# Optimization experiments

Hardware: AMD Instinct MI355X
Metric: run time of the kernel (lower is better)

The kernel has to match this reference:

```python
import jax, jax.numpy as jnp
import numpy as np

B, V, L, H, E, META = 2048, 4096, 10, 512, 256, 15
TAU = 1.2
SOS = 0
EOS = 0


def setup_inputs() -> dict:
    key = jax.random.key(0)
    ks = jax.random.split(key, 8)
    hidden_state = jax.random.normal(ks[0], (B, META), jnp.float32)
    W_in = jax.random.normal(ks[1], (META, H), jnp.float32) * 0.1
    b_in = jnp.zeros((H,), jnp.float32)
    embedding = jax.random.normal(ks[2], (V, E), jnp.float32) * 0.1
    W_ih = jax.random.normal(ks[3], (4 * H, E), jnp.float32) * (1.0 / np.sqrt(E))
    W_hh = jax.random.normal(ks[4], (4 * H, H), jnp.float32) * (1.0 / np.sqrt(H))
    b_ih = jnp.zeros((4 * H,), jnp.float32)
    # forget-gate bias initialized to 1 (reset_parameters)
    b_hh = jnp.zeros((4 * H,), jnp.float32).at[H:2 * H].set(1.0)
    W_out = jax.random.normal(ks[5], (H, V), jnp.float32) * 0.02
    b_out = jnp.zeros((V,), jnp.float32)
    u = jax.random.uniform(ks[6], (L, B, V), jnp.float32, 1e-8, 1.0 - 1e-8)
    gumbel = -jnp.log(-jnp.log(u))
    return {"hidden_state": hidden_state, "W_in": W_in, "b_in": b_in,
            "embedding": embedding, "W_ih": W_ih, "W_hh": W_hh,
            "b_ih": b_ih, "b_hh": b_hh, "W_out": W_out, "b_out": b_out,
            "gumbel": gumbel}


def reference(hidden_state, W_in, b_in, embedding, W_ih, W_hh, b_ih, b_hh,
              W_out, b_out, gumbel):
    initial_length = L + 1
    h0 = hidden_state @ W_in + b_in              # [B,H] input_module (meta)
    c0 = jnp.zeros_like(h0)
    tok0 = jnp.zeros((B, V), jnp.float32).at[:, SOS].set(1.0)  # one-hot sos
    sl0 = jnp.full((B,), initial_length, jnp.int32)

    def step(carry, xs):
        h, c, tok, sl = carry
        i, g = xs
        emb = tok @ embedding                                  # [B,E]
        gates = emb @ W_ih.T + b_ih + h @ W_hh.T + b_hh        # [B,4H]
        ig, fg, gg, og = jnp.split(gates, 4, axis=1)
        c = jax.nn.sigmoid(fg) * c + jax.nn.sigmoid(ig) * jnp.tanh(gg)
        h = jax.nn.sigmoid(og) * jnp.tanh(c)
        logits = h @ W_out + b_out                             # [B,V]
        logp = jax.nn.log_softmax(logits, axis=1)
        p = jnp.exp(logp)
        ent = -jnp.sum(p * logp, axis=1)                       # Categorical entropy
        # gumbel_softmax(p, tau, hard=True): softmax((log p + g)/tau), straight-through
        y = jax.nn.softmax((logp + g) / TAU, axis=1)
        hard = jax.nn.one_hot(jnp.argmax(y, axis=1), V, dtype=y.dtype)
        tok_new = jax.lax.stop_gradient(hard - y) + y
        mask = (hard[:, EOS] == 1.0) & (sl == initial_length)
        sl = jnp.where(mask, i + 2, sl)  # seq_pos = i+1, set to seq_pos+1
        return (h, c, tok_new, sl), (tok_new, emb, ent)

    (_, _, _, seq_lengths), (toks, embeds, ents) = jax.lax.scan(
        step, (h0, c0, tok0, sl0), (jnp.arange(L, dtype=jnp.int32), gumbel))
    output = jnp.concatenate([tok0[:, None, :], jnp.transpose(toks, (1, 0, 2))], axis=1)  # [B,L+1,V]
    embeds_out = jnp.transpose(embeds, (1, 0, 2))              # [B,L,E]
    entropy = jnp.mean(jnp.sum(ents, axis=0)) / L
    sentence_probability = jnp.zeros((B, V), jnp.float32)      # only filled in eval mode
    return output, seq_lengths, entropy, embeds_out, sentence_probability
```

## Files before the change

kernel.cpp:

```cpp
#include <hip/hip_runtime.h>
#include <hip/hip_bf16.h>
#include <math.h>

typedef unsigned short u16;
typedef __attribute__((ext_vector_type(8))) short bf16x8;
typedef __attribute__((ext_vector_type(4))) float f32x4;

#define B_    2048
#define V_    4096
#define L_    10
#define H_    512
#define E_    256
#define META_ 15
#define H4_   2048
#define EOS_  0
#define INIT_LEN_ (L_ + 1)

constexpr size_t OUT_SL  = (size_t)B_ * (L_ + 1) * V_;
constexpr size_t OUT_ENT = OUT_SL + B_;
constexpr size_t OUT_EMB = OUT_ENT + 1;
constexpr size_t OUT_SP  = OUT_EMB + (size_t)B_ * L_ * E_;

constexpr size_t WS_E2G     = 0;
constexpr size_t WS_BIG     = WS_E2G + (size_t)V_ * H4_;
constexpr size_t WS_C       = WS_BIG + (size_t)B_ * V_;
constexpr size_t WS_F32_END = WS_C + (size_t)B_ * H_;
constexpr size_t U_WOUT_HI  = 0;
constexpr size_t U_WOUT_LO  = U_WOUT_HI + (size_t)V_ * H_;
constexpr size_t U_WHH_HI   = U_WOUT_LO + (size_t)V_ * H_;
constexpr size_t U_WHH_LO   = U_WHH_HI + (size_t)H4_ * H_;
constexpr size_t U_HHI      = U_WHH_LO + (size_t)H4_ * H_;
constexpr size_t U_HLO      = U_HHI + (size_t)B_ * H_;
constexpr size_t U_END      = U_HLO + (size_t)B_ * H_;

__device__ __forceinline__ u16 f2bf(float f) {
    union { __hip_bfloat16 b; u16 u; } cv; cv.b = __float2bfloat16(f); return cv.u;
}
__device__ __forceinline__ float bf2f(u16 u) {
    union { u16 u; __hip_bfloat16 b; } cv; cv.u = u; return __bfloat162float(cv.b);
}

__device__ __forceinline__ void gld16(const u16* g, void* l) {
    __builtin_amdgcn_global_load_lds(
        (const __attribute__((address_space(1))) unsigned int*)g,
        (__attribute__((address_space(3))) unsigned int*)l, 16, 0, 0);
}

template <int EPI>
__global__ __launch_bounds__(256)
void gemm_mfma(const u16* __restrict__ Ah, const u16* __restrict__ Al,
               const u16* __restrict__ Bh, const u16* __restrict__ Bl,
               float* __restrict__ C, int N, int K,
               const float* __restrict__ bias, const int* __restrict__ tokidx,
               const float* __restrict__ e2g)
{
    __shared__ u16 As[2][128][32];
    __shared__ u16 Bs[2][128][32];
    const int tid  = threadIdx.x;
    const int lane = tid & 63;
    const int wave = tid >> 6;
    const int wm = wave >> 1, wn = wave & 1;
    const int col0 = blockIdx.x * 128;
    const int row0 = blockIdx.y * 128;

    const int srow = tid >> 2;
    const int scol = (tid & 3) * 8;
    const size_t aoff = (size_t)(row0 + srow) * K + scol;
    const size_t boff = (size_t)(col0 + srow) * K + scol;
    const size_t skip = (size_t)64 * K;

    u16* lA0 = &As[0][0][0];
    u16* lA1 = &As[1][0][0];
    u16* lB0 = &Bs[0][0][0];
    u16* lB1 = &Bs[1][0][0];
    const int d0 = tid * 8;
    const int d1 = d0 + 2048;

    f32x4 acc[4][4] = {};
    const int fr = lane & 15;
    const int kq = lane >> 4;

    for (int k0 = 0; k0 < K; k0 += 32) {
        __syncthreads();
        gld16(Ah + aoff + k0,        lA0 + d0);
        gld16(Ah + aoff + k0 + skip, lA0 + d1);
        gld16(Al + aoff + k0,        lA1 + d0);
        gld16(Al + aoff + k0 + skip, lA1 + d1);
        gld16(Bh + boff + k0,        lB0 + d0);
        gld16(Bh + boff + k0 + skip, lB0 + d1);
        gld16(Bl + boff + k0,        lB1 + d0);
        gld16(Bl + boff + k0 + skip, lB1 + d1);
        __syncthreads();

        bf16x8 ah[4], al[4], bh[4], bl[4];
#pragma unroll
        for (int i = 0; i < 4; ++i) {
            ah[i] = *(const bf16x8*)&As[0][wm * 64 + i * 16 + fr][kq * 8];
            al[i] = *(const bf16x8*)&As[1][wm * 64 + i * 16 + fr][kq * 8];
            bh[i] = *(const bf16x8*)&Bs[0][wn * 64 + i * 16 + fr][kq * 8];
            bl[i] = *(const bf16x8*)&Bs[1][wn * 64 + i * 16 + fr][kq * 8];
        }
#pragma unroll
        for (int mi = 0; mi < 4; ++mi)
#pragma unroll
            for (int ni = 0; ni < 4; ++ni) {
                acc[mi][ni] = __builtin_amdgcn_mfma_f32_16x16x32_bf16(ah[mi], bh[ni], acc[mi][ni], 0, 0, 0);
                acc[mi][ni] = __builtin_amdgcn_mfma_f32_16x16x32_bf16(ah[mi], bl[ni], acc[mi][ni], 0, 0, 0);
                acc[mi][ni] = __builtin_amdgcn_mfma_f32_16x16x32_bf16(al[mi], bh[ni], acc[mi][ni], 0, 0, 0);
            }
    }

    const int ccol = col0 + wn * 64 + fr;
#pragma unroll
    for (int mi = 0; mi < 4; ++mi) {
#pragma unroll
        for (int r = 0; r < 4; ++r) {
            const int grow = row0 + wm * 64 + mi * 16 + kq * 4 + r;
            float* cp = C + (size_t)grow * N + ccol;
            const float* ep = (EPI == 1) ? (e2g + (size_t)tokidx[grow] * H4_ + ccol)
                                         : nullptr;
#pragma unroll
            for (int ni = 0; ni < 4; ++ni) {
                float v = acc[mi][ni][r];
                if (EPI == 1) v += ep[ni * 16];
                if (EPI == 2) v += bias[ccol + ni * 16];
                cp[ni * 16] = v;
            }
        }
    }
}

template <int EPI>
__global__ __launch_bounds__(256)
void gemm_nt(const float* __restrict__ A, const float* __restrict__ Bm,
             float* __restrict__ C, int M, int N, int K,
             const float* __restrict__ bias0, const float* __restrict__ bias1)
{
    __shared__ float As[8][132];
    __shared__ float Bs[8][132];
    const int tid  = threadIdx.x;
    const int col0 = blockIdx.x * 128;
    const int row0 = blockIdx.y * 128;
    const int tx = tid & 15;
    const int ty = tid >> 4;
    const int lrow = tid >> 1;
    const int lkq  = (tid & 1) * 4;

    const float* Aptr = A + (size_t)(row0 + lrow) * K + lkq;
    const float* Bptr = Bm + (size_t)(col0 + lrow) * K + lkq;

    float acc[8][8] = {};

    for (int k0 = 0; k0 < K; k0 += 8) {
        float4 av = *(const float4*)(Aptr + k0);
        float4 bv = *(const float4*)(Bptr + k0);
        __syncthreads();
        As[lkq + 0][lrow] = av.x; As[lkq + 1][lrow] = av.y;
        As[lkq + 2][lrow] = av.z; As[lkq + 3][lrow] = av.w;
        Bs[lkq + 0][lrow] = bv.x; Bs[lkq + 1][lrow] = bv.y;
        Bs[lkq + 2][lrow] = bv.z; Bs[lkq + 3][lrow] = bv.w;
        __syncthreads();
#pragma unroll
        for (int kk = 0; kk < 8; ++kk) {
            float4 a0 = *(const float4*)&As[kk][ty * 8];
            float4 a1 = *(const float4*)&As[kk][ty * 8 + 4];
            float4 b0 = *(const float4*)&Bs[kk][tx * 8];
            float4 b1 = *(const float4*)&Bs[kk][tx * 8 + 4];
            float ar[8] = {a0.x, a0.y, a0.z, a0.w, a1.x, a1.y, a1.z, a1.w};
            float br[8] = {b0.x, b0.y, b0.z, b0.w, b1.x, b1.y, b1.z, b1.w};
#pragma unroll
            for (int r = 0; r < 8; ++r)
#pragma unroll
                for (int cc = 0; cc < 8; ++cc)
                    acc[r][cc] = fmaf(ar[r], br[cc], acc[r][cc]);
        }
    }

    const int ccol = col0 + tx * 8;
#pragma unroll
    for (int r = 0; r < 8; ++r) {
        const int grow = row0 + ty * 8 + r;
        float* cp = C + (size_t)grow * N + ccol;
#pragma unroll
        for (int cc = 0; cc < 8; ++cc) {
            float v = acc[r][cc];
            if (EPI == 0) v += bias0[ccol + cc] + bias1[ccol + cc];
            acc[r][cc] = v;
        }
        *(float4*)(cp)     = make_float4(acc[r][0], acc[r][1], acc[r][2], acc[r][3]);
        *(float4*)(cp + 4) = make_float4(acc[r][4], acc[r][5], acc[r][6], acc[r][7]);
    }
}

__global__ __launch_bounds__(256)
void split_wout(const float* __restrict__ W_out, u16* __restrict__ hiT,
                u16* __restrict__ loT)
{
    __shared__ float t[32][33];
    const int v0 = blockIdx.x * 32, k0 = blockIdx.y * 32;
    const int x = threadIdx.x & 31, y = threadIdx.x >> 5;
    for (int yy = y; yy < 32; yy += 8)
        t[yy][x] = W_out[(size_t)(k0 + yy) * V_ + v0 + x];
    __syncthreads();
    for (int yy = y; yy < 32; yy += 8) {
        const float v = t[x][yy];
        const u16 h = f2bf(v);
        hiT[(size_t)(v0 + yy) * H_ + k0 + x] = h;
        loT[(size_t)(v0 + yy) * H_ + k0 + x] = f2bf(v - bf2f(h));
    }
}

__global__ __launch_bounds__(256)
void split_mat(const float* __restrict__ X, u16* __restrict__ hi,
               u16* __restrict__ lo)
{
    const int i = blockIdx.x * 256 + threadIdx.x;
    float4 v = ((const float4*)X)[i];
    const u16 h0 = f2bf(v.x), h1 = f2bf(v.y), h2 = f2bf(v.z), h3 = f2bf(v.w);
    ((ushort4*)hi)[i] = make_ushort4(h0, h1, h2, h3);
    ((ushort4*)lo)[i] = make_ushort4(f2bf(v.x - bf2f(h0)), f2bf(v.y - bf2f(h1)),
                                     f2bf(v.z - bf2f(h2)), f2bf(v.w - bf2f(h3)));
}

__global__ __launch_bounds__(256)
void h0_kernel(const float* __restrict__ hs, const float* __restrict__ W_in,
               const float* __restrict__ b_in, u16* __restrict__ h_hi,
               u16* __restrict__ h_lo, float* __restrict__ c)
{
    const int idx = blockIdx.x * 256 + threadIdx.x;
    const int b = idx >> 9, j = idx & 511;
    float acc = b_in[j];
#pragma unroll
    for (int e = 0; e < META_; ++e)
        acc = fmaf(hs[b * META_ + e], W_in[e * H_ + j], acc);
    const u16 hh = f2bf(acc);
    h_hi[idx] = hh;
    h_lo[idx] = f2bf(acc - bf2f(hh));
    c[idx] = 0.f;
}

__global__ __launch_bounds__(256)
void init_outputs(float* __restrict__ out, int* __restrict__ tok,
                  int* __restrict__ sl, float* __restrict__ ents)
{
    const int tid = blockIdx.x * 256 + threadIdx.x;
    {
        const int b = tid >> 10;
        const int q = tid & 1023;
        float4 z = make_float4(0.f, 0.f, 0.f, 0.f);
        if (q == 0) z.x = 1.0f;
        ((float4*)out)[(size_t)b * ((L_ + 1) * V_ / 4) + q] = z;
    }
    for (size_t t = tid; t < (size_t)B_ * V_; t += (size_t)gridDim.x * 256)
        out[OUT_SP + t] = 0.f;
    if (tid < B_) { tok[tid] = 0; sl[tid] = INIT_LEN_; ents[tid] = 0.f; }
}

__global__ __launch_bounds__(256)
void lstm_cell(const float* __restrict__ gates, u16* __restrict__ h_hi,
               u16* __restrict__ h_lo, float* __restrict__ c,
               const float* __restrict__ embedding, const int* __restrict__ tok,
               float* __restrict__ out, int step)
{
    const int idx = blockIdx.x * 256 + threadIdx.x;
    const int b = idx >> 9, j = idx & 511;
    const size_t g0 = (size_t)b * H4_;
    const float ig = gates[g0 + j];
    const float fg = gates[g0 + H_ + j];
    const float gg = gates[g0 + 2 * H_ + j];
    const float og = gates[g0 + 3 * H_ + j];
    const float si = 1.f / (1.f + expf(-ig));
    const float sf = 1.f / (1.f + expf(-fg));
    const float so = 1.f / (1.f + expf(-og));
    const float cn = sf * c[idx] + si * tanhf(gg);
    c[idx] = cn;
    const float hv = so * tanhf(cn);
    const u16 hh = f2bf(hv);
    h_hi[idx] = hh;
    h_lo[idx] = f2bf(hv - bf2f(hh));
    if (j < E_)
        out[OUT_EMB + ((size_t)b * L_ + step) * E_ + j] =
            embedding[(size_t)tok[b] * E_ + j];
}

__global__ __launch_bounds__(256)
void softmax_step(const float* __restrict__ logits, const float* __restrict__ gumbel,
                  float* __restrict__ out, int* __restrict__ tok,
                  int* __restrict__ sl, float* __restrict__ ents, int step)
{
    const int b   = blockIdx.x;
    const int tid = threadIdx.x;
    const float* lrow = logits + (size_t)b * V_;
    const float* grow = gumbel + ((size_t)step * B_ + b) * V_;
    __shared__ float lsm[V_];
    __shared__ float red_m[4], red_bv[4], red_s[4], red_t[4];
    __shared__ int   red_bi[4];
    __shared__ float s_M;
    __shared__ int   s_bi;

    float m = -3.4e38f, bv = -3.4e38f;
    int bi = 0x7fffffff;
    for (int q = tid; q < V_ / 4; q += 256) {
        float4 l4 = ((const float4*)lrow)[q];
        float4 g4 = ((const float4*)grow)[q];
        ((float4*)lsm)[q] = l4;
        m = fmaxf(m, fmaxf(fmaxf(l4.x, l4.y), fmaxf(l4.z, l4.w)));
        float p; const int i4 = q * 4;
        p = l4.x + g4.x; if (p > bv) { bv = p; bi = i4; }
        p = l4.y + g4.y; if (p > bv) { bv = p; bi = i4 + 1; }
        p = l4.z + g4.z; if (p > bv) { bv = p; bi = i4 + 2; }
        p = l4.w + g4.w; if (p > bv) { bv = p; bi = i4 + 3; }
    }
#pragma unroll
    for (int off = 32; off > 0; off >>= 1) {
        m = fmaxf(m, __shfl_down(m, off));
        float obv = __shfl_down(bv, off);
        int   obi = __shfl_down(bi, off);
        if (obv > bv || (obv == bv && obi < bi)) { bv = obv; bi = obi; }
    }
    const int wave = tid >> 6, lane = tid & 63;
    if (lane == 0) { red_m[wave] = m; red_bv[wave] = bv; red_bi[wave] = bi; }
    __syncthreads();
    if (tid == 0) {
        m = red_m[0]; bv = red_bv[0]; bi = red_bi[0];
        for (int w = 1; w < 4; ++w) {
            m = fmaxf(m, red_m[w]);
            if (red_bv[w] > bv || (red_bv[w] == bv && red_bi[w] < bi)) {
                bv = red_bv[w]; bi = red_bi[w];
            }
        }
        s_M = m; s_bi = bi;
    }
    __syncthreads();
    const float M = s_M;
    const int amax = s_bi;

    float s = 0.f, t = 0.f;
    for (int q = tid; q < V_; q += 256) {
        const float l = lsm[q];
        const float e = __expf(l - M);
        s += e; t += e * l;
    }
#pragma unroll
    for (int off = 32; off > 0; off >>= 1) {
        s += __shfl_down(s, off);
        t += __shfl_down(t, off);
    }
    if (lane == 0) { red_s[wave] = s; red_t[wave] = t; }

    float* orow = out + ((size_t)b * (L_ + 1) + step + 1) * V_;
    const float4 z4 = make_float4(0.f, 0.f, 0.f, 0.f);
    for (int q = tid; q < V_ / 4; q += 256) ((float4*)orow)[q] = z4;
    __syncthreads();
    if (tid == 0) {
        const float ss = red_s[0] + red_s[1] + red_s[2] + red_s[3];
        const float tt = red_t[0] + red_t[1] + red_t[2] + red_t[3];
        const float ent = (M + logf(ss)) - tt / ss;
        ents[b] += ent;
        orow[amax] = 1.0f;
        tok[b] = amax;
        if (amax == EOS_ && sl[b] == INIT_LEN_) sl[b] = step + 2;
    }
}

__global__ __launch_bounds__(256)
void finalize(const int* __restrict__ sl, const float* __restrict__ ents,
              float* __restrict__ out)
{
    const int tid = threadIdx.x;
    float s = 0.f;
    for (int b = tid; b < B_; b += 256) {
        s += ents[b];
        out[OUT_SL + b] = (float)sl[b];
    }
    __shared__ float red[4];
#pragma unroll
    for (int off = 32; off > 0; off >>= 1) s += __shfl_down(s, off);
    if ((tid & 63) == 0) red[tid >> 6] = s;
    __syncthreads();
    if (tid == 0)
        out[OUT_ENT] = (red[0] + red[1] + red[2] + red[3]) / (float)B_ / (float)L_;
}

extern "C" void kernel_launch(void* const* d_in, const int* in_sizes, int n_in,
                              void* d_out, int out_size, void* d_ws, size_t ws_size,
                              hipStream_t stream)
{
    const float* hidden    = (const float*)d_in[0];
    const float* W_in      = (const float*)d_in[1];
    const float* b_in      = (const float*)d_in[2];
    const float* embedding = (const float*)d_in[3];
    const float* W_ih      = (const float*)d_in[4];
    const float* W_hh      = (const float*)d_in[5];
    const float* b_ih      = (const float*)d_in[6];
    const float* b_hh      = (const float*)d_in[7];
    const float* W_out     = (const float*)d_in[8];
    const float* b_out     = (const float*)d_in[9];
    const float* gumbel    = (const float*)d_in[10];
    float* out = (float*)d_out;

    float* ws    = (float*)d_ws;
    float* E2G   = ws + WS_E2G;
    float* big   = ws + WS_BIG;
    float* c     = ws + WS_C;
    u16*   wsu   = (u16*)(ws + WS_F32_END);
    u16* wout_hi = wsu + U_WOUT_HI;
    u16* wout_lo = wsu + U_WOUT_LO;
    u16* whh_hi  = wsu + U_WHH_HI;
    u16* whh_lo  = wsu + U_WHH_LO;
    u16* h_hi    = wsu + U_HHI;
    u16* h_lo    = wsu + U_HLO;
    int* tok     = (int*)(wsu + U_END);
    int* sl      = tok + B_;
    float* ents  = (float*)(sl + B_);

    split_wout<<<dim3(V_ / 32, H_ / 32), 256, 0, stream>>>(W_out, wout_hi, wout_lo);
    split_mat<<<(H4_ * H_ / 4) / 256, 256, 0, stream>>>(W_hh, whh_hi, whh_lo);
    h0_kernel<<<(B_ * H_) / 256, 256, 0, stream>>>(hidden, W_in, b_in, h_hi, h_lo, c);
    init_outputs<<<(B_ * V_ / 4) / 256, 256, 0, stream>>>(out, tok, sl, ents);
    gemm_nt<0><<<dim3(H4_ / 128, V_ / 128), 256, 0, stream>>>(
        embedding, W_ih, E2G, V_, H4_, E_, b_ih, b_hh);

    for (int i = 0; i < L_; ++i) {
        gemm_mfma<1><<<dim3(H4_ / 128, B_ / 128), 256, 0, stream>>>(
            h_hi, h_lo, whh_hi, whh_lo, big, H4_, H_, nullptr, tok, E2G);
        lstm_cell<<<(B_ * H_) / 256, 256, 0, stream>>>(big, h_hi, h_lo, c,
                                                       embedding, tok, out, i);
        gemm_mfma<2><<<dim3(V_ / 128, B_ / 128), 256, 0, stream>>>(
            h_hi, h_lo, wout_hi, wout_lo, big, V_, H_, b_out, nullptr, nullptr);
        softmax_step<<<B_, 256, 0, stream>>>(big, gumbel, out, tok, sl, ents, i);
    }
    finalize<<<1, 256, 0, stream>>>(sl, ents, out);
}
```

Measured before the change: 988.5 us.

## Fuse recurrent and output GEMMs via concatenated weights; move E2G to MFMA

```diff
diff --git a/kernel.cpp b/kernel.cpp
--- a/kernel.cpp
+++ b/kernel.cpp
@@ -13,6 +13,7 @@
 #define E_    256
 #define META_ 15
 #define H4_   2048
+#define W6_   (H4_ + V_)
 #define EOS_  0
 #define INIT_LEN_ (L_ + 1)
 
@@ -22,16 +23,15 @@
 constexpr size_t OUT_SP  = OUT_EMB + (size_t)B_ * L_ * E_;
 
 constexpr size_t WS_E2G     = 0;
-constexpr size_t WS_BIG     = WS_E2G + (size_t)V_ * H4_;
-constexpr size_t WS_C       = WS_BIG + (size_t)B_ * V_;
-constexpr size_t WS_F32_END = WS_C + (size_t)B_ * H_;
-constexpr size_t U_WOUT_HI  = 0;
-constexpr size_t U_WOUT_LO  = U_WOUT_HI + (size_t)V_ * H_;
-constexpr size_t U_WHH_HI   = U_WOUT_LO + (size_t)V_ * H_;
-constexpr size_t U_WHH_LO   = U_WHH_HI + (size_t)H4_ * H_;
-constexpr size_t U_HHI      = U_WHH_LO + (size_t)H4_ * H_;
-constexpr size_t U_HLO      = U_HHI + (size_t)B_ * H_;
-constexpr size_t U_END      = U_HLO + (size_t)B_ * H_;
+constexpr size_t WS_LOGITS  = WS_E2G    + (size_t)V_ * H4_;
+constexpr size_t WS_G       = WS_LOGITS + (size_t)B_ * V_;
+constexpr size_t WS_C       = WS_G      + (size_t)B_ * H4_;
+constexpr size_t WS_F32_END = WS_C      + (size_t)B_ * H_;
+constexpr size_t U_W6_HI    = 0;
+constexpr size_t U_W6_LO    = U_W6_HI + (size_t)W6_ * H_;
+constexpr size_t U_HHI      = U_W6_LO + (size_t)W6_ * H_;
+constexpr size_t U_HLO      = U_HHI   + (size_t)B_ * H_;
+constexpr size_t U_END      = U_HLO   + (size_t)B_ * H_;
 
 __device__ __forceinline__ u16 f2bf(float f) {
     union { __hip_bfloat16 b; u16 u; } cv; cv.b = __float2bfloat16(f); return cv.u;
@@ -48,11 +48,11 @@
 
 template <int EPI>
 __global__ __launch_bounds__(256)
-void gemm_mfma(const u16* __restrict__ Ah, const u16* __restrict__ Al,
-               const u16* __restrict__ Bh, const u16* __restrict__ Bl,
-               float* __restrict__ C, int N, int K,
-               const float* __restrict__ bias, const int* __restrict__ tokidx,
-               const float* __restrict__ e2g)
+void gemm3(const u16* __restrict__ Ah, const u16* __restrict__ Al,
+           const u16* __restrict__ Bh, const u16* __restrict__ Bl,
+           float* __restrict__ C0, float* __restrict__ C1, int K,
+           const float* __restrict__ bias0, const float* __restrict__ bias1,
+           int xoff)
 {
     __shared__ u16 As[2][128][32];
     __shared__ u16 Bs[2][128][32];
@@ -60,8 +60,14 @@
     const int lane = tid & 63;
     const int wave = tid >> 6;
     const int wm = wave >> 1, wn = wave & 1;
-    const int col0 = blockIdx.x * 128;
-    const int row0 = blockIdx.y * 128;
+
+    const int nwg  = gridDim.x * gridDim.y;
+    const int bid  = blockIdx.y * gridDim.x + blockIdx.x;
+    const int w    = (bid & 7) * (nwg >> 3) + (bid >> 3);
+    const int colb = w / gridDim.y + xoff;
+    const int rowb = w % gridDim.y;
+    const int col0 = colb * 128;
+    const int row0 = rowb * 128;
 
     const int srow = tid >> 2;
     const int scol = (tid & 3) * 8;
@@ -110,85 +116,33 @@
             }
     }
 
-    const int ccol = col0 + wn * 64 + fr;
+    const int cc0 = col0 + wn * 64 + fr;
+    float* Cbase;
+    int ldc, ccol;
+    bool addBias;
+    if (EPI == 0) {
+        Cbase = C0; ldc = H4_; ccol = cc0; addBias = true;
+    } else {
+        const bool isG = (col0 < H4_);
+        Cbase = isG ? C0 : C1;
+        ldc   = isG ? H4_ : V_;
+        ccol  = isG ? cc0 : cc0 - H4_;
+        addBias = !isG;
+    }
 #pragma unroll
     for (int mi = 0; mi < 4; ++mi) {
 #pragma unroll
         for (int r = 0; r < 4; ++r) {
             const int grow = row0 + wm * 64 + mi * 16 + kq * 4 + r;
-            float* cp = C + (size_t)grow * N + ccol;
-            const float* ep = (EPI == 1) ? (e2g + (size_t)tokidx[grow] * H4_ + ccol)
-                                         : nullptr;
+            float* cp = Cbase + (size_t)grow * ldc + ccol;
 #pragma unroll
             for (int ni = 0; ni < 4; ++ni) {
                 float v = acc[mi][ni][r];
-                if (EPI == 1) v += ep[ni * 16];
-                if (EPI == 2) v += bias[ccol + ni * 16];
+                if (EPI == 0) v += bias0[ccol + ni * 16] + bias1[ccol + ni * 16];
+                if (EPI == 1 && addBias) v += bias0[ccol + ni * 16];
                 cp[ni * 16] = v;
             }
         }
-    }
-}
-
-template <int EPI>
-__global__ __launch_bounds__(256)
-void gemm_nt(const float* __restrict__ A, const float* __restrict__ Bm,
-             float* __restrict__ C, int M, int N, int K,
-             const float* __restrict__ bias0, const float* __restrict__ bias1)
-{
-    __shared__ float As[8][132];
-    __shared__ float Bs[8][132];
-    const int tid  = threadIdx.x;
-    const int col0 = blockIdx.x * 128;
-    const int row0 = blockIdx.y * 128;
-    const int tx = tid & 15;
-    const int ty = tid >> 4;
-    const int lrow = tid >> 1;
-    const int lkq  = (tid & 1) * 4;
-
-    const float* Aptr = A + (size_t)(row0 + lrow) * K + lkq;
-    const float* Bptr = Bm + (size_t)(col0 + lrow) * K + lkq;
-
-    float acc[8][8] = {};
-
-    for (int k0 = 0; k0 < K; k0 += 8) {
-        float4 av = *(const float4*)(Aptr + k0);
-        float4 bv = *(const float4*)(Bptr + k0);
-        __syncthreads();
-        As[lkq + 0][lrow] = av.x; As[lkq + 1][lrow] = av.y;
-        As[lkq + 2][lrow] = av.z; As[lkq + 3][lrow] = av.w;
-        Bs[lkq + 0][lrow] = bv.x; Bs[lkq + 1][lrow] = bv.y;
-        Bs[lkq + 2][lrow] = bv.z; Bs[lkq + 3][lrow] = bv.w;
-        __syncthreads();
-#pragma unroll
-        for (int kk = 0; kk < 8; ++kk) {
-            float4 a0 = *(const float4*)&As[kk][ty * 8];
-            float4 a1 = *(const float4*)&As[kk][ty * 8 + 4];
-            float4 b0 = *(const float4*)&Bs[kk][tx * 8];
-            float4 b1 = *(const float4*)&Bs[kk][tx * 8 + 4];
-            float ar[8] = {a0.x, a0.y, a0.z, a0.w, a1.x, a1.y, a1.z, a1.w};
-            float br[8] = {b0.x, b0.y, b0.z, b0.w, b1.x, b1.y, b1.z, b1.w};
-#pragma unroll
-            for (int r = 0; r < 8; ++r)
-#pragma unroll
-                for (int cc = 0; cc < 8; ++cc)
-                    acc[r][cc] = fmaf(ar[r], br[cc], acc[r][cc]);
-        }
-    }
-
-    const int ccol = col0 + tx * 8;
-#pragma unroll
-    for (int r = 0; r < 8; ++r) {
-        const int grow = row0 + ty * 8 + r;
-        float* cp = C + (size_t)grow * N + ccol;
-#pragma unroll
-        for (int cc = 0; cc < 8; ++cc) {
-            float v = acc[r][cc];
-            if (EPI == 0) v += bias0[ccol + cc] + bias1[ccol + cc];
-            acc[r][cc] = v;
-        }
-        *(float4*)(cp)     = make_float4(acc[r][0], acc[r][1], acc[r][2], acc[r][3]);
-        *(float4*)(cp + 4) = make_float4(acc[r][4], acc[r][5], acc[r][6], acc[r][7]);
     }
 }
 
@@ -257,18 +211,19 @@
 }
 
 __global__ __launch_bounds__(256)
-void lstm_cell(const float* __restrict__ gates, u16* __restrict__ h_hi,
-               u16* __restrict__ h_lo, float* __restrict__ c,
-               const float* __restrict__ embedding, const int* __restrict__ tok,
-               float* __restrict__ out, int step)
+void lstm_cell(const float* __restrict__ G, const float* __restrict__ e2g,
+               u16* __restrict__ h_hi, u16* __restrict__ h_lo,
+               float* __restrict__ c, const float* __restrict__ embedding,
+               const int* __restrict__ tok, float* __restrict__ out, int step)
 {
     const int idx = blockIdx.x * 256 + threadIdx.x;
     const int b = idx >> 9, j = idx & 511;
     const size_t g0 = (size_t)b * H4_;
-    const float ig = gates[g0 + j];
-    const float fg = gates[g0 + H_ + j];
-    const float gg = gates[g0 + 2 * H_ + j];
-    const float og = gates[g0 + 3 * H_ + j];
+    const size_t e0 = (size_t)tok[b] * H4_;
+    const float ig = G[g0 + j]          + e2g[e0 + j];
+    const float fg = G[g0 + H_ + j]     + e2g[e0 + H_ + j];
+    const float gg = G[g0 + 2 * H_ + j] + e2g[e0 + 2 * H_ + j];
+    const float og = G[g0 + 3 * H_ + j] + e2g[e0 + 3 * H_ + j];
     const float si = 1.f / (1.f + expf(-ig));
     const float sf = 1.f / (1.f + expf(-fg));
     const float so = 1.f / (1.f + expf(-og));
@@ -401,34 +356,45 @@
 
     float* ws    = (float*)d_ws;
     float* E2G   = ws + WS_E2G;
-    float* big   = ws + WS_BIG;
+    float* logit = ws + WS_LOGITS;
+    float* G     = ws + WS_G;
     float* c     = ws + WS_C;
     u16*   wsu   = (u16*)(ws + WS_F32_END);
-    u16* wout_hi = wsu + U_WOUT_HI;
-    u16* wout_lo = wsu + U_WOUT_LO;
-    u16* whh_hi  = wsu + U_WHH_HI;
-    u16* whh_lo  = wsu + U_WHH_LO;
+    u16* w6_hi   = wsu + U_W6_HI;
+    u16* w6_lo   = wsu + U_W6_LO;
     u16* h_hi    = wsu + U_HHI;
     u16* h_lo    = wsu + U_HLO;
     int* tok     = (int*)(wsu + U_END);
     int* sl      = tok + B_;
     float* ents  = (float*)(sl + B_);
-
-    split_wout<<<dim3(V_ / 32, H_ / 32), 256, 0, stream>>>(W_out, wout_hi, wout_lo);
-    split_mat<<<(H4_ * H_ / 4) / 256, 256, 0, stream>>>(W_hh, whh_hi, whh_lo);
+    u16* emb_hi  = (u16*)logit;
+    u16* emb_lo  = emb_hi + (size_t)V_ * E_;
+    u16* wih_hi  = emb_lo + (size_t)V_ * E_;
+    u16* wih_lo  = wih_hi + (size_t)H4_ * E_;
+
+    split_mat<<<(H4_ * H_ / 4) / 256, 256, 0, stream>>>(W_hh, w6_hi, w6_lo);
+    split_wout<<<dim3(V_ / 32, H_ / 32), 256, 0, stream>>>(
+        W_out, w6_hi + (size_t)H4_ * H_, w6_lo + (size_t)H4_ * H_);
+    split_mat<<<(V_ * E_ / 4) / 256, 256, 0, stream>>>(embedding, emb_hi, emb_lo);
+    split_mat<<<(H4_ * E_ / 4) / 256, 256, 0, stream>>>(W_ih, wih_hi, wih_lo);
     h0_kernel<<<(B_ * H_) / 256, 256, 0, stream>>>(hidden, W_in, b_in, h_hi, h_lo, c);
     init_outputs<<<(B_ * V_ / 4) / 256, 256, 0, stream>>>(out, tok, sl, ents);
-    gemm_nt<0><<<dim3(H4_ / 128, V_ / 128), 256, 0, stream>>>(
-        embedding, W_ih, E2G, V_, H4_, E_, b_ih, b_hh);
+    gemm3<0><<<dim3(H4_ / 128, V_ / 128), 256, 0, stream>>>(
+        emb_hi, emb_lo, wih_hi, wih_lo, E2G, nullptr, E_, b_ih, b_hh, 0);
+    gemm3<1><<<dim3(H4_ / 128, B_ / 128), 256, 0, stream>>>(
+        h_hi, h_lo, w6_hi, w6_lo, G, logit, H_, b_out, nullptr, 0);
 
     for (int i = 0; i < L_; ++i) {
-        gemm_mfma<1><<<dim3(H4_ / 128, B_ / 128), 256, 0, stream>>>(
-            h_hi, h_lo, whh_hi, whh_lo, big, H4_, H_, nullptr, tok, E2G);
-        lstm_cell<<<(B_ * H_) / 256, 256, 0, stream>>>(big, h_hi, h_lo, c,
+        lstm_cell<<<(B_ * H_) / 256, 256, 0, stream>>>(G, E2G, h_hi, h_lo, c,
                                                        embedding, tok, out, i);
-        gemm_mfma<2><<<dim3(V_ / 128, B_ / 128), 256, 0, stream>>>(
-            h_hi, h_lo, wout_hi, wout_lo, big, V_, H_, b_out, nullptr, nullptr);
-        softmax_step<<<B_, 256, 0, stream>>>(big, gumbel, out, tok, sl, ents, i);
+        if (i < L_ - 1) {
+            gemm3<1><<<dim3(W6_ / 128, B_ / 128), 256, 0, stream>>>(
+                h_hi, h_lo, w6_hi, w6_lo, G, logit, H_, b_out, nullptr, 0);
+        } else {
+            gemm3<1><<<dim3(V_ / 128, B_ / 128), 256, 0, stream>>>(
+                h_hi, h_lo, w6_hi, w6_lo, G, logit, H_, b_out, nullptr, H4_ / 128);
+        }
+        softmax_step<<<B_, 256, 0, stream>>>(logit, gumbel, out, tok, sl, ents, i);
     }
     finalize<<<1, 256, 0, stream>>>(sl, ents, out);
 }
```

After: 865.1 us. 1.14x faster.
